# Kernel optimization log

Hardware: AMD Instinct MI355X
Metric: run time of the kernel (lower is better)

## Reference

```python
import jax, jax.numpy as jnp
import numpy as np

NUM_EMBEDDINGS = 1024
EMBEDDING_DIM = 128
COMMITMENT_COST = 0.25


def setup_inputs() -> dict:
    key = jax.random.key(0)
    k1, k2 = jax.random.split(key)
    z = jax.random.normal(k1, (16, EMBEDDING_DIM, 64, 64), dtype=jnp.float32)
    # torch init: uniform(-1/num_embeddings, 1/num_embeddings)
    lim = 1.0 / NUM_EMBEDDINGS
    embedding = jax.random.uniform(
        k2, (NUM_EMBEDDINGS, EMBEDDING_DIM), dtype=jnp.float32,
        minval=-lim, maxval=lim)
    return {"z": z, "embedding": embedding}


def reference(z, embedding):
    b, c, h, w = z.shape  # c == EMBEDDING_DIM
    # (b, h, w, c) -> (b*h*w, c)
    z_flat = jnp.transpose(z, (0, 2, 3, 1)).reshape(-1, c)
    # squared euclidean distances: ||z||^2 + ||e||^2 - 2 z e^T  -> (N, K)
    distances = (jnp.sum(z_flat ** 2, axis=-1, keepdims=True)
                 + jnp.sum(embedding ** 2, axis=-1)[None, :]
                 - 2.0 * jnp.matmul(z_flat, embedding.T))
    encoding_indices = jnp.argmin(distances, axis=-1)  # (N,) int
    z_q = embedding[encoding_indices].reshape(b, h, w, c)
    z_q = jnp.transpose(z_q, (0, 3, 1, 2))  # (b, c, h, w)
    commitment_loss = COMMITMENT_COST * jnp.sum(
        (jax.lax.stop_gradient(z_q) - z) ** 2)
    codebook_loss = jnp.sum((z_q - jax.lax.stop_gradient(z)) ** 2)
    loss = codebook_loss + commitment_loss
    # straight-through estimator
    z_q_st = z + jax.lax.stop_gradient(z_q - z)
    return (z_q_st, loss, encoding_indices, commitment_loss, codebook_loss)
```

## Files before the change

kernel.cpp:

```cpp
#include <hip/hip_runtime.h>
#include <hip/hip_bf16.h>

#define C 128
#define HW 4096
#define NPOS 65536
#define K 1024
#define MB 256
#define NBLK (NPOS/MB)
#define RS 136
#define RSB 272
#define CHK 128
#define NCH (K/CHK)
#define CHB (CHK*RSB)

#define ZQ_OFF 0
#define LOSS_OFF 8388608
#define IDX_OFF 8388609
#define COMMIT_OFF 8454145
#define CODE_OFF 8454146

#define WS_IMG_OFF 8192

typedef __bf16 bf16x8 __attribute__((ext_vector_type(8)));
typedef float f32x4 __attribute__((ext_vector_type(4)));
typedef unsigned short u16x8 __attribute__((ext_vector_type(8)));

__global__ void vq_prep(const float* __restrict__ emb, unsigned char* __restrict__ img,
                        float* __restrict__ S) {
    int k = blockIdx.x;
    int l = threadIdx.x;
    if (k == 0 && l == 0) { S[0] = 0.0f; ((unsigned int*)S)[1] = 0u; }
    float v0 = emb[k * C + l];
    float v1 = emb[k * C + 64 + l];
    __hip_bfloat16 h0 = __float2bfloat16(v0);
    __hip_bfloat16 h1 = __float2bfloat16(v1);
    unsigned short* row = (unsigned short*)(img + (size_t)k * RSB);
    row[l] = *(unsigned short*)&h0;
    row[64 + l] = *(unsigned short*)&h1;
    float s = v0 * v0 + v1 * v1;
    #pragma unroll
    for (int off = 32; off; off >>= 1) s += __shfl_down(s, off);
    if (l == 0) *(float*)(img + (size_t)k * RSB + 256) = s + 1.0f;
}

__global__ __launch_bounds__(512)
void vq_main(const float* __restrict__ z, const float* __restrict__ emb,
             const unsigned char* __restrict__ img,
             float* __restrict__ out, float* __restrict__ S) {
    __shared__ __align__(16) unsigned short zt[MB * RS];
    __shared__ __align__(16) unsigned short bbuf[2][CHK * RS];
    __shared__ unsigned int wbest[2][MB];
    __shared__ unsigned short idxs[MB];
    __shared__ float lred[8];

    const int t = threadIdx.x;
    const int w = t >> 6;
    const int lane = t & 63;
    const int nn = lane & 15;
    const int q = lane >> 4;
    const int wm = w >> 1;
    const int wn = w & 1;

    const int blk = blockIdx.x;
    const int n0g = blk * MB;
    const int b = n0g >> 12;
    const int hw0 = n0g & (HW - 1);
    const float* zg = z + (size_t)b * C * HW + hw0;

    for (int j = w; j < 34; j += 8) {
        __builtin_amdgcn_global_load_lds(
            (const __attribute__((address_space(1))) unsigned int*)(img + j * 1024 + lane * 16),
            (__attribute__((address_space(3))) unsigned int*)((unsigned char*)bbuf[0] + j * 1024),
            16, 0, 0);
    }

    {
        const int pos4 = (t & 63) * 4;
        const int c0 = (t >> 6) * 16;
        float4 fv[16];
        #pragma unroll
        for (int i = 0; i < 16; ++i)
            fv[i] = *(const float4*)&zg[(size_t)(c0 + i) * HW + pos4];
        #pragma unroll
        for (int j = 0; j < 4; ++j) {
            u16x8 p0, p1;
            #pragma unroll
            for (int i = 0; i < 8; ++i) {
                float f0 = (j == 0) ? fv[i].x : (j == 1) ? fv[i].y
                         : (j == 2) ? fv[i].z : fv[i].w;
                float f1 = (j == 0) ? fv[8 + i].x : (j == 1) ? fv[8 + i].y
                         : (j == 2) ? fv[8 + i].z : fv[8 + i].w;
                __hip_bfloat16 h0 = __float2bfloat16(f0);
                __hip_bfloat16 h1 = __float2bfloat16(f1);
                p0[i] = *(unsigned short*)&h0;
                p1[i] = *(unsigned short*)&h1;
            }
            *(u16x8*)&zt[(pos4 + j) * RS + c0] = p0;
            *(u16x8*)&zt[(pos4 + j) * RS + c0 + 8] = p1;
        }
    }
    __syncthreads();

    bf16x8 a[4][4];
    #pragma unroll
    for (int mt = 0; mt < 4; ++mt)
        #pragma unroll
        for (int ks = 0; ks < 4; ++ks) {
            a[mt][ks] = *(bf16x8*)&zt[(wm * 64 + mt * 16 + nn) * RS + ks * 32 + q * 8];
            asm volatile("" : "+v"(*(f32x4*)&a[mt][ks]));
        }

    unsigned int best[4][4];
    #pragma unroll
    for (int mt = 0; mt < 4; ++mt)
        #pragma unroll
        for (int r = 0; r < 4; ++r) best[mt][r] = 0xFFFFFFFFu;

    for (int ch = 0; ch < NCH; ++ch) {
        const int p = ch & 1;
        if (ch + 1 < NCH) {
            const unsigned char* src = img + (size_t)(ch + 1) * CHB;
            for (int j = w; j < 34; j += 8) {
                __builtin_amdgcn_global_load_lds(
                    (const __attribute__((address_space(1))) unsigned int*)(src + j * 1024 + lane * 16),
                    (__attribute__((address_space(3))) unsigned int*)((unsigned char*)bbuf[p ^ 1] + j * 1024),
                    16, 0, 0);
            }
        }
        const unsigned short* bb = bbuf[p];

        #pragma unroll
        for (int half = 0; half < 2; ++half) {
            const int row0 = wn * 64 + half * 32 + nn;
            const int row1 = row0 + 16;
            bf16x8 bf0[4], bf1[4];
            #pragma unroll
            for (int ks = 0; ks < 4; ++ks) {
                bf0[ks] = *(const bf16x8*)&bb[row0 * RS + ks * 32 + q * 8];
                bf1[ks] = *(const bf16x8*)&bb[row1 * RS + ks * 32 + q * 8];
            }
            const float en0 = *(const float*)&bb[row0 * RS + 128];
            const float en1 = *(const float*)&bb[row1 * RS + 128];
            const unsigned int code0 = (unsigned int)(ch * CHK + wn * 64 + half * 32 + nn);

            f32x4 acc0[4], acc1[4];
            #pragma unroll
            for (int mt = 0; mt < 4; ++mt) {
                acc0[mt] = (f32x4){0.f, 0.f, 0.f, 0.f};
                acc1[mt] = (f32x4){0.f, 0.f, 0.f, 0.f};
            }
            #pragma unroll
            for (int ks = 0; ks < 4; ++ks)
                #pragma unroll
                for (int mt = 0; mt < 4; ++mt) {
                    acc0[mt] = __builtin_amdgcn_mfma_f32_16x16x32_bf16(a[mt][ks], bf0[ks], acc0[mt], 0, 0, 0);
                    acc1[mt] = __builtin_amdgcn_mfma_f32_16x16x32_bf16(a[mt][ks], bf1[ks], acc1[mt], 0, 0, 0);
                }

            #pragma unroll
            for (int mt = 0; mt < 4; ++mt)
                #pragma unroll
                for (int r = 0; r < 4; ++r) {
                    float s0 = fmaf(acc0[mt][r], -2.0f, en0);
                    float s1 = fmaf(acc1[mt][r], -2.0f, en1);
                    unsigned int u0 = (__float_as_uint(s0) & ~1023u) | code0;
                    unsigned int u1 = (__float_as_uint(s1) & ~1023u) | (code0 + 16u);
                    best[mt][r] = min(best[mt][r], min(u0, u1));
                }
        }
        __syncthreads();
    }

    #pragma unroll
    for (int mt = 0; mt < 4; ++mt)
        #pragma unroll
        for (int r = 0; r < 4; ++r) {
            unsigned int v = best[mt][r];
            v = min(v, (unsigned int)__shfl_xor((int)v, 1));
            v = min(v, (unsigned int)__shfl_xor((int)v, 2));
            v = min(v, (unsigned int)__shfl_xor((int)v, 4));
            v = min(v, (unsigned int)__shfl_xor((int)v, 8));
            if (nn == 0) wbest[wn][wm * 64 + mt * 16 + q * 4 + r] = v;
        }
    __syncthreads();

    if (t < MB) {
        unsigned int v = min(wbest[0][t], wbest[1][t]);
        unsigned int code = v & 1023u;
        idxs[t] = (unsigned short)code;
        out[IDX_OFF + n0g + t] = (float)code;
    }
    __syncthreads();

    {
        const int pos4 = (t & 63) * 4;
        const int c0 = (t >> 6) * 16;
        float* og = out + ZQ_OFF + (size_t)b * C * HW + hw0;
        float ev[4][16];
        float ls = 0.f;
        #pragma unroll
        for (int j = 0; j < 4; ++j) {
            const int pos = pos4 + j;
            const float* erow = emb + (size_t)idxs[pos] * C;
            #pragma unroll
            for (int g = 0; g < 4; ++g) {
                float4 e = *(const float4*)&erow[c0 + g * 4];
                ev[j][g * 4 + 0] = e.x; ev[j][g * 4 + 1] = e.y;
                ev[j][g * 4 + 2] = e.z; ev[j][g * 4 + 3] = e.w;
            }
            u16x8 z0 = *(u16x8*)&zt[pos * RS + c0];
            u16x8 z1 = *(u16x8*)&zt[pos * RS + c0 + 8];
            #pragma unroll
            for (int i = 0; i < 8; ++i) {
                float zf0 = __uint_as_float((unsigned int)z0[i] << 16);
                float zf1 = __uint_as_float((unsigned int)z1[i] << 16);
                float d0 = zf0 - ev[j][i];
                float d1 = zf1 - ev[j][8 + i];
                ls += d0 * d0 + d1 * d1;
            }
        }
        #pragma unroll
        for (int i = 0; i < 16; ++i) {
            float4 v = { ev[0][i], ev[1][i], ev[2][i], ev[3][i] };
            *(float4*)&og[(size_t)(c0 + i) * HW + pos4] = v;
        }
        #pragma unroll
        for (int off = 32; off; off >>= 1) ls += __shfl_down(ls, off);
        if (lane == 0) lred[w] = ls;
    }
    __syncthreads();

    if (t == 0) {
        float bs = 0.f;
        #pragma unroll
        for (int i = 0; i < 8; ++i) bs += lred[i];
        float prev = atomicAdd(S, bs);
        asm volatile("" :: "v"(prev) : "memory");
        unsigned int old = atomicAdd((unsigned int*)S + 1, 1u);
        if (old == NBLK - 1) {
            float s = atomicAdd(S, 0.0f);
            out[LOSS_OFF] = 1.25f * s;
            out[COMMIT_OFF] = 0.25f * s;
            out[CODE_OFF] = s;
        }
    }
}

extern "C" void kernel_launch(void* const* d_in, const int* in_sizes, int n_in,
                              void* d_out, int out_size, void* d_ws, size_t ws_size,
                              hipStream_t stream) {
    const float* z = (const float*)d_in[0];
    const float* emb = (const float*)d_in[1];
    float* out = (float*)d_out;
    float* S = (float*)d_ws;
    unsigned char* img = (unsigned char*)d_ws + WS_IMG_OFF;

    vq_prep<<<K, 64, 0, stream>>>(emb, img, S);
    vq_main<<<NBLK, 512, 0, stream>>>(z, emb, img, out, S);
}
```

Before: 117.7 us.

## Keep codebook slice resident in registers per wave, stream z tiles from LDS

Each of the 8 waves now holds a fixed 128-code slice of the bf16 codebook in registers for the whole block, and loops over all 16 position tiles read from LDS. This replaces the previous loop that streamed 128-code chunks through double-buffered LDS with per-chunk barriers. The per-wave minima go into an 8-way wbest array and are reduced at the end. The change removes the chunk pipeline and its barriers and frees the LDS codebook buffers, at the cost of about 128 extra VGPRs for the B fragments and an LDS read of the z fragments for every tile.

```diff
diff --git a/kernel.cpp b/kernel.cpp
--- a/kernel.cpp
+++ b/kernel.cpp
@@ -9,9 +9,6 @@
 #define NBLK (NPOS/MB)
 #define RS 136
 #define RSB 272
-#define CHK 128
-#define NCH (K/CHK)
-#define CHB (CHK*RSB)
 
 #define ZQ_OFF 0
 #define LOSS_OFF 8388608
@@ -20,6 +17,8 @@
 #define CODE_OFF 8454146
 
 #define WS_IMG_OFF 8192
+
+#define ZT_PAD 2048
 
 typedef __bf16 bf16x8 __attribute__((ext_vector_type(8)));
 typedef float f32x4 __attribute__((ext_vector_type(4)));
@@ -47,9 +46,8 @@
 void vq_main(const float* __restrict__ z, const float* __restrict__ emb,
              const unsigned char* __restrict__ img,
              float* __restrict__ out, float* __restrict__ S) {
-    __shared__ __align__(16) unsigned short zt[MB * RS];
-    __shared__ __align__(16) unsigned short bbuf[2][CHK * RS];
-    __shared__ unsigned int wbest[2][MB];
+    __shared__ __align__(16) unsigned short zt[MB * RS + ZT_PAD];
+    __shared__ unsigned int wbest[8][MB];
     __shared__ unsigned short idxs[MB];
     __shared__ float lred[8];
 
@@ -58,8 +56,7 @@
     const int lane = t & 63;
     const int nn = lane & 15;
     const int q = lane >> 4;
-    const int wm = w >> 1;
-    const int wn = w & 1;
+    const int wbase = w * 128;
 
     const int blk = blockIdx.x;
     const int n0g = blk * MB;
@@ -67,125 +64,94 @@
     const int hw0 = n0g & (HW - 1);
     const float* zg = z + (size_t)b * C * HW + hw0;
 
-    for (int j = w; j < 34; j += 8) {
-        __builtin_amdgcn_global_load_lds(
-            (const __attribute__((address_space(1))) unsigned int*)(img + j * 1024 + lane * 16),
-            (__attribute__((address_space(3))) unsigned int*)((unsigned char*)bbuf[0] + j * 1024),
-            16, 0, 0);
-    }
-
-    {
-        const int pos4 = (t & 63) * 4;
-        const int c0 = (t >> 6) * 16;
-        float4 fv[16];
-        #pragma unroll
-        for (int i = 0; i < 16; ++i)
-            fv[i] = *(const float4*)&zg[(size_t)(c0 + i) * HW + pos4];
-        #pragma unroll
-        for (int j = 0; j < 4; ++j) {
-            u16x8 p0, p1;
-            #pragma unroll
-            for (int i = 0; i < 8; ++i) {
-                float f0 = (j == 0) ? fv[i].x : (j == 1) ? fv[i].y
-                         : (j == 2) ? fv[i].z : fv[i].w;
-                float f1 = (j == 0) ? fv[8 + i].x : (j == 1) ? fv[8 + i].y
-                         : (j == 2) ? fv[8 + i].z : fv[8 + i].w;
-                __hip_bfloat16 h0 = __float2bfloat16(f0);
-                __hip_bfloat16 h1 = __float2bfloat16(f1);
-                p0[i] = *(unsigned short*)&h0;
-                p1[i] = *(unsigned short*)&h1;
+    const int pos4 = (t & 63) * 4;
+    const int c0 = (t >> 6) * 16;
+    float4 fv[16];
+    #pragma unroll
+    for (int i = 0; i < 16; ++i)
+        fv[i] = *(const float4*)&zg[(size_t)(c0 + i) * HW + pos4];
+
+    bf16x8 bp[8][4];
+    float en[8];
+    #pragma unroll
+    for (int nt = 0; nt < 8; ++nt) {
+        const unsigned char* rowp = img + (size_t)(wbase + nt * 16 + nn) * RSB;
+        #pragma unroll
+        for (int ks = 0; ks < 4; ++ks)
+            bp[nt][ks] = *(const bf16x8*)(rowp + ks * 64 + q * 16);
+        en[nt] = *(const float*)(rowp + 256);
+    }
+    #pragma unroll
+    for (int nt = 0; nt < 8; ++nt) {
+        #pragma unroll
+        for (int ks = 0; ks < 4; ++ks)
+            asm volatile("" : "+v"(*(f32x4*)&bp[nt][ks]));
+        asm volatile("" : "+v"(en[nt]));
+    }
+
+    #pragma unroll
+    for (int j = 0; j < 4; ++j) {
+        u16x8 p0, p1;
+        #pragma unroll
+        for (int i = 0; i < 8; ++i) {
+            float f0 = (j == 0) ? fv[i].x : (j == 1) ? fv[i].y
+                     : (j == 2) ? fv[i].z : fv[i].w;
+            float f1 = (j == 0) ? fv[8 + i].x : (j == 1) ? fv[8 + i].y
+                     : (j == 2) ? fv[8 + i].z : fv[8 + i].w;
+            __hip_bfloat16 h0 = __float2bfloat16(f0);
+            __hip_bfloat16 h1 = __float2bfloat16(f1);
+            p0[i] = *(unsigned short*)&h0;
+            p1[i] = *(unsigned short*)&h1;
+        }
+        *(u16x8*)&zt[(pos4 + j) * RS + c0] = p0;
+        *(u16x8*)&zt[(pos4 + j) * RS + c0 + 8] = p1;
+    }
+    __syncthreads();
+
+    const int mt0 = (w * 2) & 15;
+    for (int i = 0; i < 16; ++i) {
+        const int mt = (mt0 + i) & 15;
+        bf16x8 zf[4];
+        #pragma unroll
+        for (int ks = 0; ks < 4; ++ks)
+            zf[ks] = *(bf16x8*)&zt[(mt * 16 + nn) * RS + ks * 32 + q * 8];
+
+        f32x4 acc[8];
+        #pragma unroll
+        for (int nt = 0; nt < 8; ++nt) acc[nt] = (f32x4){0.f, 0.f, 0.f, 0.f};
+        #pragma unroll
+        for (int ks = 0; ks < 4; ++ks)
+            #pragma unroll
+            for (int nt = 0; nt < 8; ++nt)
+                acc[nt] = __builtin_amdgcn_mfma_f32_16x16x32_bf16(zf[ks], bp[nt][ks], acc[nt], 0, 0, 0);
+
+        unsigned int best4[4] = {0xFFFFFFFFu, 0xFFFFFFFFu, 0xFFFFFFFFu, 0xFFFFFFFFu};
+        #pragma unroll
+        for (int nt = 0; nt < 8; ++nt) {
+            const unsigned int codent = (unsigned int)(wbase + nt * 16 + nn);
+            #pragma unroll
+            for (int r = 0; r < 4; ++r) {
+                float s = fmaf(acc[nt][r], -2.0f, en[nt]);
+                unsigned int u = (__float_as_uint(s) & ~1023u) | codent;
+                best4[r] = min(best4[r], u);
             }
-            *(u16x8*)&zt[(pos4 + j) * RS + c0] = p0;
-            *(u16x8*)&zt[(pos4 + j) * RS + c0 + 8] = p1;
-        }
-    }
-    __syncthreads();
-
-    bf16x8 a[4][4];
-    #pragma unroll
-    for (int mt = 0; mt < 4; ++mt)
-        #pragma unroll
-        for (int ks = 0; ks < 4; ++ks) {
-            a[mt][ks] = *(bf16x8*)&zt[(wm * 64 + mt * 16 + nn) * RS + ks * 32 + q * 8];
-            asm volatile("" : "+v"(*(f32x4*)&a[mt][ks]));
-        }
-
-    unsigned int best[4][4];
-    #pragma unroll
-    for (int mt = 0; mt < 4; ++mt)
-        #pragma unroll
-        for (int r = 0; r < 4; ++r) best[mt][r] = 0xFFFFFFFFu;
-
-    for (int ch = 0; ch < NCH; ++ch) {
-        const int p = ch & 1;
-        if (ch + 1 < NCH) {
-            const unsigned char* src = img + (size_t)(ch + 1) * CHB;
-            for (int j = w; j < 34; j += 8) {
-                __builtin_amdgcn_global_load_lds(
-                    (const __attribute__((address_space(1))) unsigned int*)(src + j * 1024 + lane * 16),
-                    (__attribute__((address_space(3))) unsigned int*)((unsigned char*)bbuf[p ^ 1] + j * 1024),
-                    16, 0, 0);
-            }
-        }
-        const unsigned short* bb = bbuf[p];
-
-        #pragma unroll
-        for (int half = 0; half < 2; ++half) {
-            const int row0 = wn * 64 + half * 32 + nn;
-            const int row1 = row0 + 16;
-            bf16x8 bf0[4], bf1[4];
-            #pragma unroll
-            for (int ks = 0; ks < 4; ++ks) {
-                bf0[ks] = *(const bf16x8*)&bb[row0 * RS + ks * 32 + q * 8];
-                bf1[ks] = *(const bf16x8*)&bb[row1 * RS + ks * 32 + q * 8];
-            }
-            const float en0 = *(const float*)&bb[row0 * RS + 128];
-            const float en1 = *(const float*)&bb[row1 * RS + 128];
-            const unsigned int code0 = (unsigned int)(ch * CHK + wn * 64 + half * 32 + nn);
-
-            f32x4 acc0[4], acc1[4];
-            #pragma unroll
-            for (int mt = 0; mt < 4; ++mt) {
-                acc0[mt] = (f32x4){0.f, 0.f, 0.f, 0.f};
-                acc1[mt] = (f32x4){0.f, 0.f, 0.f, 0.f};
-            }
-            #pragma unroll
-            for (int ks = 0; ks < 4; ++ks)
-                #pragma unroll
-                for (int mt = 0; mt < 4; ++mt) {
-                    acc0[mt] = __builtin_amdgcn_mfma_f32_16x16x32_bf16(a[mt][ks], bf0[ks], acc0[mt], 0, 0, 0);
-                    acc1[mt] = __builtin_amdgcn_mfma_f32_16x16x32_bf16(a[mt][ks], bf1[ks], acc1[mt], 0, 0, 0);
-                }
-
-            #pragma unroll
-            for (int mt = 0; mt < 4; ++mt)
-                #pragma unroll
-                for (int r = 0; r < 4; ++r) {
-                    float s0 = fmaf(acc0[mt][r], -2.0f, en0);
-                    float s1 = fmaf(acc1[mt][r], -2.0f, en1);
-                    unsigned int u0 = (__float_as_uint(s0) & ~1023u) | code0;
-                    unsigned int u1 = (__float_as_uint(s1) & ~1023u) | (code0 + 16u);
-                    best[mt][r] = min(best[mt][r], min(u0, u1));
-                }
-        }
-        __syncthreads();
-    }
-
-    #pragma unroll
-    for (int mt = 0; mt < 4; ++mt)
+        }
         #pragma unroll
         for (int r = 0; r < 4; ++r) {
-            unsigned int v = best[mt][r];
+            unsigned int v = best4[r];
             v = min(v, (unsigned int)__shfl_xor((int)v, 1));
             v = min(v, (unsigned int)__shfl_xor((int)v, 2));
             v = min(v, (unsigned int)__shfl_xor((int)v, 4));
             v = min(v, (unsigned int)__shfl_xor((int)v, 8));
-            if (nn == 0) wbest[wn][wm * 64 + mt * 16 + q * 4 + r] = v;
-        }
+            if (nn == 0) wbest[w][mt * 16 + q * 4 + r] = v;
+        }
+    }
     __syncthreads();
 
     if (t < MB) {
-        unsigned int v = min(wbest[0][t], wbest[1][t]);
+        unsigned int v = wbest[0][t];
+        #pragma unroll
+        for (int i = 1; i < 8; ++i) v = min(v, wbest[i][t]);
         unsigned int code = v & 1023u;
         idxs[t] = (unsigned short)code;
         out[IDX_OFF + n0g + t] = (float)code;
@@ -193,8 +159,6 @@
     __syncthreads();
 
     {
-        const int pos4 = (t & 63) * 4;
-        const int c0 = (t >> 6) * 16;
         float* og = out + ZQ_OFF + (size_t)b * C * HW + hw0;
         float ev[4][16];
         float ls = 0.f;
```

Result: slower. 120.2 us (+2.1%).
